# Kernel optimization log

Measured on AMD Instinct MI355X. Metric: run time of the kernel, lower is better.

Reference implementation:

```python
import jax, jax.numpy as jnp
import numpy as np

IN_FEATURES = 256
OUT_FEATURES = 256
GRID_SIZE = 5
SPLINE_ORDER = 3  # k


def setup_inputs() -> dict:
    key = jax.random.key(0)
    k1, k2, k3, k4 = jax.random.split(key, 4)
    x = jax.random.uniform(k1, (1024, IN_FEATURES), dtype=jnp.float32)  # in [0,1) subset of grid_range
    base_weight = jax.random.normal(k2, (IN_FEATURES, OUT_FEATURES), dtype=jnp.float32) * 0.05
    n_basis = GRID_SIZE + SPLINE_ORDER - 1  # 7
    spline_weight = jax.random.normal(k3, (IN_FEATURES, OUT_FEATURES, n_basis), dtype=jnp.float32) * 0.05
    # grid: (grid_size, in_features); sorted per feature inside grid_range (-1,1)
    grid = jnp.sort(jax.random.uniform(k4, (GRID_SIZE, IN_FEATURES), dtype=jnp.float32, minval=-1.0, maxval=1.0), axis=0)
    return {"x": x, "base_weight": base_weight, "spline_weight": spline_weight, "grid": grid}


def _safe_div(num, den):
    # B-spline convention: 0/0 terms contribute 0 (repeated knots from constant-fill grid extension).
    ok = den != 0
    return jnp.where(ok, num / jnp.where(ok, den, 1.0), 0.0)


def _bspline_basis(x, grid, k):
    # x: (b, in); grid: (G, in) -> basis (b, in, G+k-1) via Cox-de Boor recursion.
    gt = grid.T  # (in, G)
    left = jnp.repeat(2.0 * gt[:, :1] - gt[:, k:k + 1], k, axis=1)       # k copies of 2*g0 - g_k
    right = jnp.repeat(2.0 * gt[:, -1:] - gt[:, -k - 1:-k], k, axis=1)   # k copies of 2*g_-1 - g_{-k-1}
    eg = jnp.concatenate([left, gt, right], axis=1)  # (in, G+2k) extended grid
    xe = x[:, :, None]  # (b, in, 1)
    B = ((xe >= eg[None, :, :-1]) & (xe < eg[None, :, 1:])).astype(x.dtype)  # order-1 indicator basis
    for d in range(1, k):
        lt = _safe_div(xe - eg[None, :, :-d - 1], (eg[:, d:-1] - eg[:, :-d - 1])[None])
        rt = _safe_div(eg[None, :, d + 1:] - xe, (eg[:, d + 1:] - eg[:, 1:-d])[None])
        B = lt * B[..., :-1] + rt * B[..., 1:]
    return B[..., :grid.shape[0] + k - 1]  # first G+k-1 functions, matching spline_weight's last dim


def reference(x, base_weight, spline_weight, grid):
    k = SPLINE_ORDER
    basis = _bspline_basis(x, grid, k)                     # (b, in, K)
    base_out = x @ base_weight                             # (b, out)
    spline_out = jnp.einsum('bik,iok->bio', basis, spline_weight)  # (b, in, out)
    # base_out (b,out) broadcasts against (b,in,out), as in the original tf code
    return jax.nn.silu(base_out[:, None, :] + spline_out)
```

## Files before the change

### kernel.cpp

```cpp
#include <hip/hip_runtime.h>
#include <math.h>


#define NF 256
#define BROWS 4
#define G 4

typedef float f32x4 __attribute__((ext_vector_type(4)));

__device__ __forceinline__ float silu_f(float z) {
    float e = __expf(-z);
    return z * __builtin_amdgcn_rcpf(1.0f + e);
}

__global__ __launch_bounds__(512, 2) void kan_fused(const float* __restrict__ x,
                                                    const float* __restrict__ W,
                                                    const float* __restrict__ sw,
                                                    const float* __restrict__ grid,
                                                    float* __restrict__ out) {
    const int b0 = blockIdx.x * BROWS;
    const int tid = threadIdx.x;

    __shared__ float xs[BROWS][NF];
    __shared__ float base_s[BROWS][NF];
    __shared__ float bas[BROWS][NF][8];

    if (tid < 256) {
        const int row = tid >> 6;
        const int c4 = (tid & 63) * 4;
        *reinterpret_cast<f32x4*>(&xs[row][c4]) =
            *reinterpret_cast<const f32x4*>(&x[(size_t)(b0 + row) * NF + c4]);
    }
    __syncthreads();

    {
        const int o = tid & 255;
        const int h = tid >> 8;
        float acc0 = 0.f, acc1 = 0.f;
#pragma unroll 16
        for (int k = 0; k < NF; ++k) {
            const float w = W[k * NF + o];
            acc0 += xs[2 * h + 0][k] * w;
            acc1 += xs[2 * h + 1][k] * w;
        }
        base_s[2 * h + 0][o] = acc0;
        base_s[2 * h + 1][o] = acc1;
    }

    {
        const int i = tid & 255;
        const int hh = tid >> 8;
        const float g0 = grid[0 * NF + i];
        const float g1 = grid[1 * NF + i];
        const float g2 = grid[2 * NF + i];
        const float g3 = grid[3 * NF + i];
        const float g4 = grid[4 * NF + i];
        const float L = 2.f * g0 - g3;
        const float R = 2.f * g4 - g1;
        const float eg[11] = {L, L, L, g0, g1, g2, g3, g4, R, R, R};

#pragma unroll
        for (int rep = 0; rep < 2; ++rep) {
            const int bb = hh + 2 * rep;
            const float xv = xs[bb][i];

            float B0[10];
#pragma unroll
            for (int t = 0; t < 10; ++t)
                B0[t] = (xv >= eg[t] && xv < eg[t + 1]) ? 1.f : 0.f;
            float B1[9];
#pragma unroll
            for (int t = 0; t < 9; ++t) {
                const float dl = eg[t + 1] - eg[t];
                const float dr = eg[t + 2] - eg[t + 1];
                const float lt = (dl != 0.f) ? (xv - eg[t]) / dl : 0.f;
                const float rt = (dr != 0.f) ? (eg[t + 2] - xv) / dr : 0.f;
                B1[t] = lt * B0[t] + rt * B0[t + 1];
            }
            float B2[8];
#pragma unroll
            for (int t = 0; t < 8; ++t) {
                const float dl = eg[t + 2] - eg[t];
                const float dr = eg[t + 3] - eg[t + 1];
                const float lt = (dl != 0.f) ? (xv - eg[t]) / dl : 0.f;
                const float rt = (dr != 0.f) ? (eg[t + 3] - xv) / dr : 0.f;
                B2[t] = lt * B1[t] + rt * B1[t + 1];
            }
#pragma unroll
            for (int k = 0; k < 7; ++k) bas[bb][i][k] = B2[k];
            bas[bb][i][7] = 0.f;
        }
    }
    __syncthreads();

    const int lane = tid & 63;
    const int wv = tid >> 6;
    const int o4 = lane * 4;

    f32x4 bs[BROWS];
#pragma unroll
    for (int bb = 0; bb < BROWS; ++bb)
        bs[bb] = *reinterpret_cast<const f32x4*>(&base_s[bb][o4]);

    for (int gs = 0; gs < NF / (8 * G); ++gs) {
        f32x4 q[G][7];
#pragma unroll
        for (int j = 0; j < G; ++j) {
            const int i = (gs * G + j) * 8 + wv;
            const f32x4* p4 =
                reinterpret_cast<const f32x4*>(&sw[((size_t)i * NF + o4) * 7]);
#pragma unroll
            for (int kk = 0; kk < 7; ++kk) q[j][kk] = p4[kk];
        }

#pragma unroll
        for (int bb = 0; bb < BROWS; ++bb) {
#pragma unroll
            for (int j = 0; j < G; ++j) {
                const int i = (gs * G + j) * 8 + wv;
                const f32x4 bl = *reinterpret_cast<const f32x4*>(&bas[bb][i][0]);
                const f32x4 bh = *reinterpret_cast<const f32x4*>(&bas[bb][i][4]);
                const float bk[7] = {bl.x, bl.y, bl.z, bl.w, bh.x, bh.y, bh.z};
                float s[28];
#pragma unroll
                for (int m = 0; m < 7; ++m) {
                    s[m * 4 + 0] = q[j][m].x;
                    s[m * 4 + 1] = q[j][m].y;
                    s[m * 4 + 2] = q[j][m].z;
                    s[m * 4 + 3] = q[j][m].w;
                }
                float a0 = bs[bb].x, a1 = bs[bb].y, a2 = bs[bb].z, a3 = bs[bb].w;
#pragma unroll
                for (int k = 0; k < 7; ++k) {
                    a0 += bk[k] * s[0 * 7 + k];
                    a1 += bk[k] * s[1 * 7 + k];
                    a2 += bk[k] * s[2 * 7 + k];
                    a3 += bk[k] * s[3 * 7 + k];
                }
                f32x4 o4v;
                o4v.x = silu_f(a0);
                o4v.y = silu_f(a1);
                o4v.z = silu_f(a2);
                o4v.w = silu_f(a3);
                *reinterpret_cast<f32x4*>(
                    &out[((size_t)(b0 + bb) * NF + i) * NF + o4]) = o4v;
            }
        }
    }
}

extern "C" void kernel_launch(void* const* d_in, const int* in_sizes, int n_in,
                              void* d_out, int out_size, void* d_ws, size_t ws_size,
                              hipStream_t stream) {
    const float* x    = (const float*)d_in[0];
    const float* bw   = (const float*)d_in[1];
    const float* sw   = (const float*)d_in[2];
    const float* grid = (const float*)d_in[3];
    float* out = (float*)d_out;

    kan_fused<<<dim3(256), 512, 0, stream>>>(x, bw, sw, grid, out);
}
```

Before: 74.15 us.

## Split base GEMM into separate kernel and tile main kernel over input features

Moves the x@W base projection into its own kernel that writes to workspace, then runs the spline/SiLU kernel on a 2x256 grid of 256-thread blocks, each covering 128 input features and 4 batch rows. This removes the per-block redundant-free but serial GEMM prologue from the main kernel and doubles the block count. The spline-weight loop is restructured into a software-pipelined prefetch of the next input feature's weights with each wave owning 32 contiguous features. It adds a second launch and a global round-trip for the base output.

```diff
diff --git a/kernel.cpp b/kernel.cpp
--- a/kernel.cpp
+++ b/kernel.cpp
@@ -3,8 +3,6 @@
 
 
 #define NF 256
-#define BROWS 4
-#define G 4
 
 typedef float f32x4 __attribute__((ext_vector_type(4)));
 
@@ -13,43 +11,57 @@
     return z * __builtin_amdgcn_rcpf(1.0f + e);
 }
 
-__global__ __launch_bounds__(512, 2) void kan_fused(const float* __restrict__ x,
-                                                    const float* __restrict__ W,
-                                                    const float* __restrict__ sw,
-                                                    const float* __restrict__ grid,
-                                                    float* __restrict__ out) {
-    const int b0 = blockIdx.x * BROWS;
-    const int tid = threadIdx.x;
-
-    __shared__ float xs[BROWS][NF];
-    __shared__ float base_s[BROWS][NF];
-    __shared__ float bas[BROWS][NF][8];
-
-    if (tid < 256) {
-        const int row = tid >> 6;
-        const int c4 = (tid & 63) * 4;
+__global__ __launch_bounds__(256) void base_gemm(const float* __restrict__ x,
+                                                 const float* __restrict__ W,
+                                                 float* __restrict__ base) {
+    __shared__ float xs[4][NF];
+    const int b0 = blockIdx.x * 4;
+    const int t = threadIdx.x;
+    {
+        const int row = t >> 6;
+        const int c4 = (t & 63) * 4;
         *reinterpret_cast<f32x4*>(&xs[row][c4]) =
             *reinterpret_cast<const f32x4*>(&x[(size_t)(b0 + row) * NF + c4]);
     }
     __syncthreads();
+    float acc0 = 0.f, acc1 = 0.f, acc2 = 0.f, acc3 = 0.f;
+#pragma unroll 8
+    for (int k = 0; k < NF; ++k) {
+        float w = W[k * NF + t];
+        acc0 += xs[0][k] * w;
+        acc1 += xs[1][k] * w;
+        acc2 += xs[2][k] * w;
+        acc3 += xs[3][k] * w;
+    }
+    base[(size_t)(b0 + 0) * NF + t] = acc0;
+    base[(size_t)(b0 + 1) * NF + t] = acc1;
+    base[(size_t)(b0 + 2) * NF + t] = acc2;
+    base[(size_t)(b0 + 3) * NF + t] = acc3;
+}
+
+__global__ __launch_bounds__(256) void kan_main(const float* __restrict__ x,
+                                                const float* __restrict__ sw,
+                                                const float* __restrict__ grid,
+                                                const float* __restrict__ base,
+                                                float* __restrict__ out) {
+    const int i_base = blockIdx.x * 128;
+    const int b0 = blockIdx.y * 4;
+    const int tid = threadIdx.x;
+
+    __shared__ float bas[4][128][8];
+    __shared__ float base_s[4][NF];
 
     {
-        const int o = tid & 255;
-        const int h = tid >> 8;
-        float acc0 = 0.f, acc1 = 0.f;
-#pragma unroll 16
-        for (int k = 0; k < NF; ++k) {
-            const float w = W[k * NF + o];
-            acc0 += xs[2 * h + 0][k] * w;
-            acc1 += xs[2 * h + 1][k] * w;
-        }
-        base_s[2 * h + 0][o] = acc0;
-        base_s[2 * h + 1][o] = acc1;
+        const int row = tid >> 6;
+        const int c4 = (tid & 63) * 4;
+        *reinterpret_cast<f32x4*>(&base_s[row][c4]) =
+            *reinterpret_cast<const f32x4*>(&base[(size_t)(b0 + row) * NF + c4]);
     }
 
     {
-        const int i = tid & 255;
-        const int hh = tid >> 8;
+        const int il = tid & 127;
+        const int bbh = tid >> 7;
+        const int i = i_base + il;
         const float g0 = grid[0 * NF + i];
         const float g1 = grid[1 * NF + i];
         const float g2 = grid[2 * NF + i];
@@ -61,8 +73,8 @@
 
 #pragma unroll
         for (int rep = 0; rep < 2; ++rep) {
-            const int bb = hh + 2 * rep;
-            const float xv = xs[bb][i];
+            const int bb = bbh + 2 * rep;
+            const float xv = x[(size_t)(b0 + bb) * NF + i];
 
             float B0[10];
 #pragma unroll
@@ -87,8 +99,8 @@
                 B2[t] = lt * B1[t] + rt * B1[t + 1];
             }
 #pragma unroll
-            for (int k = 0; k < 7; ++k) bas[bb][i][k] = B2[k];
-            bas[bb][i][7] = 0.f;
+            for (int k = 0; k < 7; ++k) bas[bb][il][k] = B2[k];
+            bas[bb][il][7] = 0.f;
         }
     }
     __syncthreads();
@@ -97,55 +109,67 @@
     const int wv = tid >> 6;
     const int o4 = lane * 4;
 
-    f32x4 bs[BROWS];
+    f32x4 bs[4];
 #pragma unroll
-    for (int bb = 0; bb < BROWS; ++bb)
+    for (int bb = 0; bb < 4; ++bb)
         bs[bb] = *reinterpret_cast<const f32x4*>(&base_s[bb][o4]);
 
-    for (int gs = 0; gs < NF / (8 * G); ++gs) {
-        f32x4 q[G][7];
+    const int il0 = wv * 32;
+
+    f32x4 q[7];
+    {
+        const f32x4* p4 = reinterpret_cast<const f32x4*>(
+            &sw[((size_t)(i_base + il0) * NF + o4) * 7]);
 #pragma unroll
-        for (int j = 0; j < G; ++j) {
-            const int i = (gs * G + j) * 8 + wv;
-            const f32x4* p4 =
-                reinterpret_cast<const f32x4*>(&sw[((size_t)i * NF + o4) * 7]);
+        for (int m = 0; m < 7; ++m) q[m] = p4[m];
+    }
+
+#pragma unroll 2
+    for (int t = 0; t < 32; ++t) {
+        const int il = il0 + t;
+        const int i = i_base + il;
+
+        f32x4 qn[7];
+        if (t < 31) {
+            const f32x4* p4 = reinterpret_cast<const f32x4*>(
+                &sw[((size_t)(i + 1) * NF + o4) * 7]);
 #pragma unroll
-            for (int kk = 0; kk < 7; ++kk) q[j][kk] = p4[kk];
+            for (int m = 0; m < 7; ++m) qn[m] = p4[m];
+        }
+
+        float s[28];
+#pragma unroll
+        for (int m = 0; m < 7; ++m) {
+            s[m * 4 + 0] = q[m].x;
+            s[m * 4 + 1] = q[m].y;
+            s[m * 4 + 2] = q[m].z;
+            s[m * 4 + 3] = q[m].w;
         }
 
 #pragma unroll
-        for (int bb = 0; bb < BROWS; ++bb) {
+        for (int bb = 0; bb < 4; ++bb) {
+            const f32x4 bl = *reinterpret_cast<const f32x4*>(&bas[bb][il][0]);
+            const f32x4 bh = *reinterpret_cast<const f32x4*>(&bas[bb][il][4]);
+            const float bk[7] = {bl.x, bl.y, bl.z, bl.w, bh.x, bh.y, bh.z};
+            float a0 = bs[bb].x, a1 = bs[bb].y, a2 = bs[bb].z, a3 = bs[bb].w;
 #pragma unroll
-            for (int j = 0; j < G; ++j) {
-                const int i = (gs * G + j) * 8 + wv;
-                const f32x4 bl = *reinterpret_cast<const f32x4*>(&bas[bb][i][0]);
-                const f32x4 bh = *reinterpret_cast<const f32x4*>(&bas[bb][i][4]);
-                const float bk[7] = {bl.x, bl.y, bl.z, bl.w, bh.x, bh.y, bh.z};
-                float s[28];
+            for (int k = 0; k < 7; ++k) {
+                a0 += bk[k] * s[0 * 7 + k];
+                a1 += bk[k] * s[1 * 7 + k];
+                a2 += bk[k] * s[2 * 7 + k];
+                a3 += bk[k] * s[3 * 7 + k];
+            }
+            f32x4 ov;
+            ov.x = silu_f(a0);
+            ov.y = silu_f(a1);
+            ov.z = silu_f(a2);
+            ov.w = silu_f(a3);
+            *reinterpret_cast<f32x4*>(
+                &out[((size_t)(b0 + bb) * NF + i) * NF + o4]) = ov;
+        }
+
 #pragma unroll
-                for (int m = 0; m < 7; ++m) {
-                    s[m * 4 + 0] = q[j][m].x;
-                    s[m * 4 + 1] = q[j][m].y;
-                    s[m * 4 + 2] = q[j][m].z;
-                    s[m * 4 + 3] = q[j][m].w;
-                }
-                float a0 = bs[bb].x, a1 = bs[bb].y, a2 = bs[bb].z, a3 = bs[bb].w;
-#pragma unroll
-                for (int k = 0; k < 7; ++k) {
-                    a0 += bk[k] * s[0 * 7 + k];
-                    a1 += bk[k] * s[1 * 7 + k];
-                    a2 += bk[k] * s[2 * 7 + k];
-                    a3 += bk[k] * s[3 * 7 + k];
-                }
-                f32x4 o4v;
-                o4v.x = silu_f(a0);
-                o4v.y = silu_f(a1);
-                o4v.z = silu_f(a2);
-                o4v.w = silu_f(a3);
-                *reinterpret_cast<f32x4*>(
-                    &out[((size_t)(b0 + bb) * NF + i) * NF + o4]) = o4v;
-            }
-        }
+        for (int m = 0; m < 7; ++m) q[m] = qn[m];
     }
 }
 
@@ -157,6 +181,8 @@
     const float* sw   = (const float*)d_in[2];
     const float* grid = (const float*)d_in[3];
     float* out = (float*)d_out;
+    float* base = (float*)d_ws;
 
-    kan_fused<<<dim3(256), 512, 0, stream>>>(x, bw, sw, grid, out);
+    base_gemm<<<dim3(256), 256, 0, stream>>>(x, bw, base);
+    kan_main<<<dim3(2, 256), 256, 0, stream>>>(x, sw, grid, base, out);
 }
```

Result: slower. 89.19 us (+20.3%).
